# Kernel tuning notes

Measured on AMD Instinct MI355X. Metric: run time of the kernel, lower is better.

## Reference

```python
import jax, jax.numpy as jnp
import numpy as np

EMBED = 1024
HEADS = 16
HEAD_DIM = EMBED // HEADS
N, SEQ = 8, 1024


def setup_inputs() -> dict:
    key = jax.random.key(0)
    ks = jax.random.split(key, 9)
    values = jax.random.normal(ks[0], (N, SEQ, EMBED), dtype=jnp.float32)
    keys_ = jax.random.normal(ks[1], (N, SEQ, EMBED), dtype=jnp.float32)
    query = jax.random.normal(ks[2], (N, SEQ, EMBED), dtype=jnp.float32)
    mask = jax.random.randint(ks[3], (N, 1, SEQ, SEQ), 0, 2, dtype=jnp.int32)
    s = 1.0 / np.sqrt(HEAD_DIM)
    Wv = jax.random.normal(ks[4], (HEAD_DIM, HEAD_DIM), dtype=jnp.float32) * s
    Wk = jax.random.normal(ks[5], (HEAD_DIM, HEAD_DIM), dtype=jnp.float32) * s
    Wq = jax.random.normal(ks[6], (HEAD_DIM, HEAD_DIM), dtype=jnp.float32) * s
    Wo = jax.random.normal(ks[7], (EMBED, EMBED), dtype=jnp.float32) * (1.0 / np.sqrt(EMBED))
    bo = jax.random.normal(ks[8], (EMBED,), dtype=jnp.float32) * 0.01
    return {"values": values, "keys": keys_, "query": query, "mask": mask,
            "Wv": Wv, "Wk": Wk, "Wq": Wq, "Wo": Wo, "bo": bo}


def reference(values, keys, query, mask, Wv, Wk, Wq, Wo, bo):
    n, q_len = query.shape[0], query.shape[1]
    v_len, k_len = values.shape[1], keys.shape[1]
    # reshape to (N, len, H, Dh); per-head linear projections share a (Dh,Dh) weight.
    v = values.reshape(n, v_len, HEADS, HEAD_DIM)
    k = keys.reshape(n, k_len, HEADS, HEAD_DIM)
    q = query.reshape(n, q_len, HEADS, HEAD_DIM)
    # torch Linear: x @ W.T
    v = jnp.einsum('nlhd,ed->nlhe', v, Wv)
    k = jnp.einsum('nlhd,ed->nlhe', k, Wk)
    q = jnp.einsum('nlhd,ed->nlhe', q, Wq)
    # scores (N,H,Q,K); mask BEFORE scaling, exactly as the torch module does
    att = jnp.einsum('nqhd,nkhd->nhqk', q, k)
    att = jnp.where(mask == 0, jnp.float32(-1e20), att)
    att = jax.nn.softmax(att / jnp.sqrt(jnp.float32(EMBED)), axis=3)
    out = jnp.einsum('nhql,nlhd->nqhd', att, v).reshape(n, q_len, EMBED)
    return out @ Wo.T + bo
```

## Files before the change

kernel.cpp:

```cpp
#include <hip/hip_runtime.h>
#include <hip/hip_bf16.h>

using bf16x8 = __attribute__((ext_vector_type(8))) __bf16;
using f32x4  = __attribute__((ext_vector_type(4))) float;

#define NB 8
#define SEQ 1024
#define HEADS 16
#define HD 64
#define EMB 1024

#if __has_builtin(__builtin_amdgcn_exp2f)
  #define EXPD(x) __builtin_amdgcn_exp2f(x)
  #define QSCALE  0.04508422f
  #define MASKV  -4.5084e18f
#else
  #define EXPD(x) __expf(x)
  #define QSCALE  0.03125f
  #define MASKV  -3.125e18f
#endif

__global__ __launch_bounds__(256) void mask_pack(const int* __restrict__ mask,
                                                 unsigned long long* __restrict__ mp)
{
    const int row = blockIdx.x, n = blockIdx.y, t = threadIdx.x;
    const int w = t >> 6, lane = t & 63;
    const int* m = mask + ((size_t)n * SEQ + row) * SEQ;
    #pragma unroll
    for (int i = 0; i < 4; ++i) {
        unsigned long long b = __ballot(m[i * 256 + w * 64 + lane] != 0);
        if (lane == 0) mp[((size_t)n * SEQ + row) * 16 + i * 4 + w] = b;
    }
}

__global__ __launch_bounds__(256, 4) void proj_mfma(
    const float* __restrict__ q_in, const float* __restrict__ k_in, const float* __restrict__ v_in,
    const float* __restrict__ Wq, const float* __restrict__ Wk, const float* __restrict__ Wv,
    __bf16* __restrict__ qp, __bf16* __restrict__ kp, __bf16* __restrict__ vpt)
{
    const int z = blockIdx.z;
    const float* X  = (z == 0) ? q_in : (z == 1) ? k_in : v_in;
    const float* Wf = (z == 0) ? Wq   : (z == 1) ? Wk   : Wv;

    __shared__ __align__(16) __bf16 Wb[64 * 72];
    __shared__ __align__(16) __bf16 Xb[64 * 72];
    const int t = threadIdx.x;
    const int nh = blockIdx.y, n = nh >> 4, h = nh & 15;
    const int l0 = blockIdx.x * 64;
    for (int i = t; i < 4096; i += 256)
        Wb[(i >> 6) * 72 + (i & 63)] = (__bf16)Wf[i];
    {
        const int row = t >> 2, seg = (t & 3) * 16;
        const float* src = X + ((size_t)(n * SEQ + l0 + row)) * EMB + h * 64 + seg;
        union { __bf16 b[16]; uint4 u[2]; } tmp;
        #pragma unroll
        for (int jj = 0; jj < 4; ++jj) {
            float4 f = ((const float4*)src)[jj];
            tmp.b[jj*4+0] = (__bf16)f.x; tmp.b[jj*4+1] = (__bf16)f.y;
            tmp.b[jj*4+2] = (__bf16)f.z; tmp.b[jj*4+3] = (__bf16)f.w;
        }
        *(uint4*)&Xb[row * 72 + seg]     = tmp.u[0];
        *(uint4*)&Xb[row * 72 + seg + 8] = tmp.u[1];
    }
    __syncthreads();
    const int w = t >> 6, lane = t & 63, quad = lane >> 4, lr = lane & 15;
    bf16x8 af[2];
    #pragma unroll
    for (int ks = 0; ks < 2; ++ks)
        af[ks] = *(const bf16x8*)&Xb[(w * 16 + lr) * 72 + ks * 32 + quad * 8];
    const f32x4 zero4 = {0.f, 0.f, 0.f, 0.f};
    f32x4 acc[4];
    #pragma unroll
    for (int et = 0; et < 4; ++et) {
        acc[et] = zero4;
        #pragma unroll
        for (int ks = 0; ks < 2; ++ks) {
            bf16x8 bfrag = *(const bf16x8*)&Wb[(et * 16 + lr) * 72 + ks * 32 + quad * 8];
            acc[et] = __builtin_amdgcn_mfma_f32_16x16x32_bf16(af[ks], bfrag, acc[et], 0, 0, 0);
        }
    }
    if (z == 0) {
        #pragma unroll
        for (int et = 0; et < 4; ++et) acc[et] *= QSCALE;
    }
    __syncthreads();
    if (z < 2) {
        #pragma unroll
        for (int et = 0; et < 4; ++et)
            #pragma unroll
            for (int rr = 0; rr < 4; ++rr)
                Xb[(w * 16 + quad * 4 + rr) * 72 + et * 16 + lr] = (__bf16)acc[et][rr];
        __syncthreads();
        const int row = t >> 2, seg = (t & 3) * 16;
        uint4 a = *(uint4*)&Xb[row * 72 + seg];
        uint4 b = *(uint4*)&Xb[row * 72 + seg + 8];
        __bf16* outp = (z == 0) ? qp : kp;
        __bf16* dst = outp + (size_t)nh * 65536 + (size_t)(l0 + row) * 64 + seg;
        *(uint4*)&dst[0] = a;
        *(uint4*)&dst[8] = b;
    } else {
        #pragma unroll
        for (int et = 0; et < 4; ++et)
            #pragma unroll
            for (int rr = 0; rr < 4; ++rr)
                Xb[(et * 16 + lr) * 72 + w * 16 + quad * 4 + rr] = (__bf16)acc[et][rr];
        __syncthreads();
        const int e = t >> 2, seg = (t & 3) * 16;
        uint4 a = *(uint4*)&Xb[e * 72 + seg];
        uint4 b = *(uint4*)&Xb[e * 72 + seg + 8];
        __bf16* dst = vpt + (size_t)nh * 65536 + (size_t)e * SEQ + l0 + seg;
        *(uint4*)&dst[0] = a;
        *(uint4*)&dst[8] = b;
    }
}

__global__ __launch_bounds__(256, 4) void attn_mfma(
    const __bf16* __restrict__ qp, const __bf16* __restrict__ kp, const __bf16* __restrict__ vpt,
    const unsigned long long* __restrict__ mp, __bf16* __restrict__ attn_out)
{
    __shared__ __align__(16) __bf16 Ks[64 * 72];
    __shared__ __align__(16) __bf16 Vt[64 * 72];
    __shared__ __align__(16) __bf16 Ps[4][2][16 * 72];
    const int t = threadIdx.x, w = t >> 6, lane = t & 63, quad = lane >> 4, lr = lane & 15;
    const int bid = blockIdx.x;
    const int nh = bid & 127, qg = bid >> 7;
    const int n = nh >> 4, h = nh & 15;
    const int q0 = qg * 128;
    const __bf16* Q  = qp  + (size_t)nh * 65536;
    const __bf16* K  = kp  + (size_t)nh * 65536;
    const __bf16* VT = vpt + (size_t)nh * 65536;

    int qrow[2];
    bf16x8 qf[2][2];
    const unsigned long long* mrow[2];
    #pragma unroll
    for (int g = 0; g < 2; ++g) {
        qrow[g] = q0 + g * 64 + w * 16 + lr;
        qf[g][0] = *(const bf16x8*)&Q[(size_t)qrow[g] * 64 + quad * 8];
        qf[g][1] = *(const bf16x8*)&Q[(size_t)qrow[g] * 64 + 32 + quad * 8];
        mrow[g] = mp + ((size_t)n * SEQ + qrow[g]) * 16;
    }

    const f32x4 zero4 = {0.f, 0.f, 0.f, 0.f};
    f32x4 O[2][4];
    #pragma unroll
    for (int g = 0; g < 2; ++g)
        #pragma unroll
        for (int mt = 0; mt < 4; ++mt) O[g][mt] = zero4;
    float l_part[2] = {0.f, 0.f};

    for (int kc = 0; kc < 16; ++kc) {
        __syncthreads();
        for (int c = t; c < 512; c += 256) {
            int row = c >> 3, c8 = c & 7;
            *(uint4*)&Ks[row * 72 + c8 * 8] =
                *(const uint4*)&K[(size_t)(kc * 64 + row) * 64 + c8 * 8];
            *(uint4*)&Vt[row * 72 + c8 * 8] =
                *(const uint4*)&VT[(size_t)row * SEQ + kc * 64 + c8 * 8];
        }
        const unsigned long long mw0 = mrow[0][kc], mw1 = mrow[1][kc];
        __syncthreads();
        #pragma unroll
        for (int g = 0; g < 2; ++g) {
            f32x4 S[4];
            #pragma unroll
            for (int kt = 0; kt < 4; ++kt) {
                S[kt] = zero4;
                #pragma unroll
                for (int ks = 0; ks < 2; ++ks) {
                    bf16x8 kf = *(const bf16x8*)&Ks[(kt * 16 + lr) * 72 + ks * 32 + quad * 8];
                    S[kt] = __builtin_amdgcn_mfma_f32_16x16x32_bf16(kf, qf[g][ks], S[kt], 0, 0, 0);
                }
            }
            const unsigned long long mword = g ? mw1 : mw0;
            const unsigned int mlo = (unsigned int)(mword >> (quad * 4));
            const unsigned int mhi = (unsigned int)(mword >> (32 + quad * 4));
            float lsum = 0.f;
            __bf16 pb[16];
            #pragma unroll
            for (int kt = 0; kt < 4; ++kt)
                #pragma unroll
                for (int r = 0; r < 4; ++r) {
                    unsigned int bits = (kt < 2) ? mlo : mhi;
                    int sh = (kt & 1) * 16 + r;
                    float sv = ((bits >> sh) & 1u) ? S[kt][r] : MASKV;
                    float ev = EXPD(sv);
                    lsum += ev;
                    pb[kt * 4 + r] = (__bf16)ev;
                }
            l_part[g] += lsum;
            #pragma unroll
            for (int kt = 0; kt < 4; ++kt) {
                union { __bf16 b[4]; uint2 u; } pk;
                #pragma unroll
                for (int r = 0; r < 4; ++r) pk.b[r] = pb[kt * 4 + r];
                *(uint2*)&Ps[w][g][lr * 72 + kt * 16 + quad * 4] = pk.u;
            }
        }
        __asm__ __volatile__("s_waitcnt lgkmcnt(0)" ::: "memory");
        #pragma unroll
        for (int ks = 0; ks < 2; ++ks) {
            bf16x8 pf0 = *(const bf16x8*)&Ps[w][0][lr * 72 + ks * 32 + quad * 8];
            bf16x8 pf1 = *(const bf16x8*)&Ps[w][1][lr * 72 + ks * 32 + quad * 8];
            #pragma unroll
            for (int mt = 0; mt < 4; ++mt) {
                bf16x8 vf = *(const bf16x8*)&Vt[(mt * 16 + lr) * 72 + ks * 32 + quad * 8];
                O[0][mt] = __builtin_amdgcn_mfma_f32_16x16x32_bf16(vf, pf0, O[0][mt], 0, 0, 0);
                O[1][mt] = __builtin_amdgcn_mfma_f32_16x16x32_bf16(vf, pf1, O[1][mt], 0, 0, 0);
            }
        }
    }
    #pragma unroll
    for (int g = 0; g < 2; ++g) {
        float l = l_part[g];
        l += __shfl_xor(l, 16, 64);
        l += __shfl_xor(l, 32, 64);
        const float linv = 1.0f / l;
        #pragma unroll
        for (int mt = 0; mt < 4; ++mt) {
            union { __bf16 b[4]; uint2 u; } pk;
            #pragma unroll
            for (int r = 0; r < 4; ++r) pk.b[r] = (__bf16)(O[g][mt][r] * linv);
            *(uint2*)&attn_out[((size_t)n * SEQ + qrow[g]) * EMB + h * 64 + mt * 16 + quad * 4] = pk.u;
        }
    }
}

__global__ __launch_bounds__(256) void cvt_wo(const float* __restrict__ Wo, __bf16* __restrict__ Wob)
{
    int i = blockIdx.x * 256 + threadIdx.x;
    float4 f = *(const float4*)&Wo[(size_t)i * 4];
    union { __bf16 b[4]; uint2 u; } tmp;
    tmp.b[0] = (__bf16)f.x; tmp.b[1] = (__bf16)f.y; tmp.b[2] = (__bf16)f.z; tmp.b[3] = (__bf16)f.w;
    *(uint2*)&Wob[(size_t)i * 4] = tmp.u;
}

__global__ __launch_bounds__(256, 4) void out_gemm_mfma(
    const __bf16* __restrict__ A, const __bf16* __restrict__ B,
    const float* __restrict__ bo, float* __restrict__ out)
{
    __shared__ __align__(16) __bf16 As[64 * 40];
    __shared__ __align__(16) __bf16 Bs[128 * 40];
    const int t = threadIdx.x, w = t >> 6, lane = t & 63, quad = lane >> 4, lr = lane & 15;
    const int wr = (w >> 1) * 32, wc = (w & 1) * 64;
    const int r0 = blockIdx.y * 64, e0 = blockIdx.x * 128;
    const f32x4 zero4 = {0.f, 0.f, 0.f, 0.f};
    f32x4 acc[2][4];
    #pragma unroll
    for (int mt = 0; mt < 2; ++mt)
        #pragma unroll
        for (int nt = 0; nt < 4; ++nt) acc[mt][nt] = zero4;
    for (int k0 = 0; k0 < 1024; k0 += 32) {
        __syncthreads();
        {
            int row = t >> 2, c8 = t & 3;
            *(uint4*)&As[row * 40 + c8 * 8] =
                *(const uint4*)&A[(size_t)(r0 + row) * EMB + k0 + c8 * 8];
        }
        for (int c = t; c < 512; c += 256) {
            int row = c >> 2, c8 = c & 3;
            *(uint4*)&Bs[row * 40 + c8 * 8] =
                *(const uint4*)&B[(size_t)(e0 + row) * EMB + k0 + c8 * 8];
        }
        __syncthreads();
        bf16x8 af[2], bf[4];
        #pragma unroll
        for (int mt = 0; mt < 2; ++mt)
            af[mt] = *(const bf16x8*)&As[(wr + mt * 16 + lr) * 40 + quad * 8];
        #pragma unroll
        for (int nt = 0; nt < 4; ++nt)
            bf[nt] = *(const bf16x8*)&Bs[(wc + nt * 16 + lr) * 40 + quad * 8];
        #pragma unroll
        for (int mt = 0; mt < 2; ++mt)
            #pragma unroll
            for (int nt = 0; nt < 4; ++nt)
                acc[mt][nt] = __builtin_amdgcn_mfma_f32_16x16x32_bf16(af[mt], bf[nt], acc[mt][nt], 0, 0, 0);
    }
    float bv[4];
    #pragma unroll
    for (int nt = 0; nt < 4; ++nt) bv[nt] = bo[e0 + wc + nt * 16 + lr];
    #pragma unroll
    for (int mt = 0; mt < 2; ++mt)
        #pragma unroll
        for (int nt = 0; nt < 4; ++nt)
            #pragma unroll
            for (int rr = 0; rr < 4; ++rr)
                out[(size_t)(r0 + wr + mt * 16 + quad * 4 + rr) * EMB + e0 + wc + nt * 16 + lr] =
                    acc[mt][nt][rr] + bv[nt];
}

extern "C" void kernel_launch(void* const* d_in, const int* in_sizes, int n_in,
                              void* d_out, int out_size, void* d_ws, size_t ws_size,
                              hipStream_t stream) {
    const float* values = (const float*)d_in[0];
    const float* keys   = (const float*)d_in[1];
    const float* query  = (const float*)d_in[2];
    const int*   mask   = (const int*)d_in[3];
    const float* Wv     = (const float*)d_in[4];
    const float* Wk     = (const float*)d_in[5];
    const float* Wq     = (const float*)d_in[6];
    const float* Wo     = (const float*)d_in[7];
    const float* bo     = (const float*)d_in[8];
    float* out = (float*)d_out;

    const size_t per = (size_t)NB * HEADS * SEQ * HD;
    __bf16* qp   = (__bf16*)d_ws;
    __bf16* kp   = qp + per;
    __bf16* vpt  = kp + per;
    __bf16* attn = vpt + per;
    __bf16* Wob  = attn + (size_t)NB * SEQ * EMB;
    unsigned long long* maskp = (unsigned long long*)(Wob + (size_t)EMB * EMB);

    mask_pack<<<dim3(SEQ, NB), 256, 0, stream>>>(mask, maskp);
    proj_mfma<<<dim3(16, 128, 3), 256, 0, stream>>>(query, keys, values, Wq, Wk, Wv, qp, kp, vpt);
    cvt_wo<<<1024, 256, 0, stream>>>(Wo, Wob);
    attn_mfma<<<1024, 256, 0, stream>>>(qp, kp, vpt, maskp, attn);
    out_gemm_mfma<<<dim3(EMB / 128, NB * SEQ / 64), 256, 0, stream>>>(attn, Wob, bo, out);
}
```

Baseline: 284.7 us.

## Merge prep kernels, read K/V directly from global, enlarge output GEMM tile

Folds the mask-packing and Wo bf16 conversion into one launch, which removes one kernel launch. The attention kernel no longer stages K and V tiles in shared memory and drops the two block barriers per chunk. Each wave now loads its MFMA fragments straight from global memory and depends on L1/L2 for reuse across waves. The output GEMM tile grows to 128x128 with a 4x4 accumulator per wave and unpadded LDS rows. That gives more reuse per block but costs more registers, lower occupancy, and possible LDS bank conflicts.

New measurement: 351.8 us. 23.6% more time.

```diff
diff --git a/kernel.cpp b/kernel.cpp
--- a/kernel.cpp
+++ b/kernel.cpp
@@ -20,16 +20,28 @@
   #define MASKV  -3.125e18f
 #endif
 
-__global__ __launch_bounds__(256) void mask_pack(const int* __restrict__ mask,
-                                                 unsigned long long* __restrict__ mp)
+__global__ __launch_bounds__(256) void prep_kernel(const int* __restrict__ mask,
+                                                   unsigned long long* __restrict__ mp,
+                                                   const float* __restrict__ Wo,
+                                                   __bf16* __restrict__ Wob)
 {
-    const int row = blockIdx.x, n = blockIdx.y, t = threadIdx.x;
-    const int w = t >> 6, lane = t & 63;
-    const int* m = mask + ((size_t)n * SEQ + row) * SEQ;
-    #pragma unroll
-    for (int i = 0; i < 4; ++i) {
-        unsigned long long b = __ballot(m[i * 256 + w * 64 + lane] != 0);
-        if (lane == 0) mp[((size_t)n * SEQ + row) * 16 + i * 4 + w] = b;
+    const int bid = blockIdx.x, t = threadIdx.x;
+    if (bid < NB * SEQ) {
+        const int n = bid & 7, row = bid >> 3;
+        const int w = t >> 6, lane = t & 63;
+        const int* m = mask + ((size_t)n * SEQ + row) * SEQ;
+        #pragma unroll
+        for (int i = 0; i < 4; ++i) {
+            unsigned long long b = __ballot(m[i * 256 + w * 64 + lane] != 0);
+            if (lane == 0) mp[((size_t)n * SEQ + row) * 16 + i * 4 + w] = b;
+        }
+    } else {
+        const size_t i = (size_t)(bid - NB * SEQ) * 256 + t;
+        float4 f = *(const float4*)&Wo[i * 4];
+        union { __bf16 b[4]; uint2 u; } tmp;
+        tmp.b[0] = (__bf16)f.x; tmp.b[1] = (__bf16)f.y;
+        tmp.b[2] = (__bf16)f.z; tmp.b[3] = (__bf16)f.w;
+        *(uint2*)&Wob[i * 4] = tmp.u;
     }
 }
 
@@ -118,8 +130,6 @@
     const __bf16* __restrict__ qp, const __bf16* __restrict__ kp, const __bf16* __restrict__ vpt,
     const unsigned long long* __restrict__ mp, __bf16* __restrict__ attn_out)
 {
-    __shared__ __align__(16) __bf16 Ks[64 * 72];
-    __shared__ __align__(16) __bf16 Vt[64 * 72];
     __shared__ __align__(16) __bf16 Ps[4][2][16 * 72];
     const int t = threadIdx.x, w = t >> 6, lane = t & 63, quad = lane >> 4, lr = lane & 15;
     const int bid = blockIdx.x;
@@ -150,35 +160,24 @@
     float l_part[2] = {0.f, 0.f};
 
     for (int kc = 0; kc < 16; ++kc) {
-        __syncthreads();
-        for (int c = t; c < 512; c += 256) {
-            int row = c >> 3, c8 = c & 7;
-            *(uint4*)&Ks[row * 72 + c8 * 8] =
-                *(const uint4*)&K[(size_t)(kc * 64 + row) * 64 + c8 * 8];
-            *(uint4*)&Vt[row * 72 + c8 * 8] =
-                *(const uint4*)&VT[(size_t)row * SEQ + kc * 64 + c8 * 8];
-        }
-        const unsigned long long mw0 = mrow[0][kc], mw1 = mrow[1][kc];
-        __syncthreads();
         #pragma unroll
         for (int g = 0; g < 2; ++g) {
             f32x4 S[4];
             #pragma unroll
             for (int kt = 0; kt < 4; ++kt) {
-                S[kt] = zero4;
-                #pragma unroll
-                for (int ks = 0; ks < 2; ++ks) {
-                    bf16x8 kf = *(const bf16x8*)&Ks[(kt * 16 + lr) * 72 + ks * 32 + quad * 8];
-                    S[kt] = __builtin_amdgcn_mfma_f32_16x16x32_bf16(kf, qf[g][ks], S[kt], 0, 0, 0);
-                }
+                const __bf16* kb = &K[(size_t)(kc * 64 + kt * 16 + lr) * 64 + quad * 8];
+                bf16x8 kf0 = *(const bf16x8*)&kb[0];
+                bf16x8 kf1 = *(const bf16x8*)&kb[32];
+                S[kt] = __builtin_amdgcn_mfma_f32_16x16x32_bf16(kf0, qf[g][0], zero4, 0, 0, 0);
+                S[kt] = __builtin_amdgcn_mfma_f32_16x16x32_bf16(kf1, qf[g][1], S[kt], 0, 0, 0);
             }
-            const unsigned long long mword = g ? mw1 : mw0;
+            const unsigned long long mword = mrow[g][kc];
             const unsigned int mlo = (unsigned int)(mword >> (quad * 4));
             const unsigned int mhi = (unsigned int)(mword >> (32 + quad * 4));
             float lsum = 0.f;
-            __bf16 pb[16];
-            #pragma unroll
-            for (int kt = 0; kt < 4; ++kt)
+            #pragma unroll
+            for (int kt = 0; kt < 4; ++kt) {
+                union { __bf16 b[4]; uint2 u; } pk;
                 #pragma unroll
                 for (int r = 0; r < 4; ++r) {
                     unsigned int bits = (kt < 2) ? mlo : mhi;
@@ -186,16 +185,11 @@
                     float sv = ((bits >> sh) & 1u) ? S[kt][r] : MASKV;
                     float ev = EXPD(sv);
                     lsum += ev;
-                    pb[kt * 4 + r] = (__bf16)ev;
+                    pk.b[r] = (__bf16)ev;
                 }
-            l_part[g] += lsum;
-            #pragma unroll
-            for (int kt = 0; kt < 4; ++kt) {
-                union { __bf16 b[4]; uint2 u; } pk;
-                #pragma unroll
-                for (int r = 0; r < 4; ++r) pk.b[r] = pb[kt * 4 + r];
                 *(uint2*)&Ps[w][g][lr * 72 + kt * 16 + quad * 4] = pk.u;
             }
+            l_part[g] += lsum;
         }
         __asm__ __volatile__("s_waitcnt lgkmcnt(0)" ::: "memory");
         #pragma unroll
@@ -204,7 +198,7 @@
             bf16x8 pf1 = *(const bf16x8*)&Ps[w][1][lr * 72 + ks * 32 + quad * 8];
             #pragma unroll
             for (int mt = 0; mt < 4; ++mt) {
-                bf16x8 vf = *(const bf16x8*)&Vt[(mt * 16 + lr) * 72 + ks * 32 + quad * 8];
+                bf16x8 vf = *(const bf16x8*)&VT[(size_t)(mt * 16 + lr) * SEQ + kc * 64 + ks * 32 + quad * 8];
                 O[0][mt] = __builtin_amdgcn_mfma_f32_16x16x32_bf16(vf, pf0, O[0][mt], 0, 0, 0);
                 O[1][mt] = __builtin_amdgcn_mfma_f32_16x16x32_bf16(vf, pf1, O[1][mt], 0, 0, 0);
             }
@@ -226,52 +220,41 @@
     }
 }
 
-__global__ __launch_bounds__(256) void cvt_wo(const float* __restrict__ Wo, __bf16* __restrict__ Wob)
-{
-    int i = blockIdx.x * 256 + threadIdx.x;
-    float4 f = *(const float4*)&Wo[(size_t)i * 4];
-    union { __bf16 b[4]; uint2 u; } tmp;
-    tmp.b[0] = (__bf16)f.x; tmp.b[1] = (__bf16)f.y; tmp.b[2] = (__bf16)f.z; tmp.b[3] = (__bf16)f.w;
-    *(uint2*)&Wob[(size_t)i * 4] = tmp.u;
-}
-
-__global__ __launch_bounds__(256, 4) void out_gemm_mfma(
+__global__ __launch_bounds__(256, 2) void out_gemm_mfma(
     const __bf16* __restrict__ A, const __bf16* __restrict__ B,
     const float* __restrict__ bo, float* __restrict__ out)
 {
-    __shared__ __align__(16) __bf16 As[64 * 40];
-    __shared__ __align__(16) __bf16 Bs[128 * 40];
+    __shared__ __align__(16) __bf16 As[128 * 32];
+    __shared__ __align__(16) __bf16 Bs[128 * 32];
     const int t = threadIdx.x, w = t >> 6, lane = t & 63, quad = lane >> 4, lr = lane & 15;
-    const int wr = (w >> 1) * 32, wc = (w & 1) * 64;
-    const int r0 = blockIdx.y * 64, e0 = blockIdx.x * 128;
+    const int wr = (w >> 1) * 64, wc = (w & 1) * 64;
+    const int r0 = blockIdx.y * 128, e0 = blockIdx.x * 128;
     const f32x4 zero4 = {0.f, 0.f, 0.f, 0.f};
-    f32x4 acc[2][4];
-    #pragma unroll
-    for (int mt = 0; mt < 2; ++mt)
+    f32x4 acc[4][4];
+    #pragma unroll
+    for (int mt = 0; mt < 4; ++mt)
         #pragma unroll
         for (int nt = 0; nt < 4; ++nt) acc[mt][nt] = zero4;
     for (int k0 = 0; k0 < 1024; k0 += 32) {
         __syncthreads();
-        {
-            int row = t >> 2, c8 = t & 3;
-            *(uint4*)&As[row * 40 + c8 * 8] =
-                *(const uint4*)&A[(size_t)(r0 + row) * EMB + k0 + c8 * 8];
-        }
+        #pragma unroll
         for (int c = t; c < 512; c += 256) {
-            int row = c >> 2, c8 = c & 3;
-            *(uint4*)&Bs[row * 40 + c8 * 8] =
-                *(const uint4*)&B[(size_t)(e0 + row) * EMB + k0 + c8 * 8];
+            int row = c >> 2, seg = c & 3;
+            *(uint4*)&As[row * 32 + seg * 8] =
+                *(const uint4*)&A[(size_t)(r0 + row) * EMB + k0 + seg * 8];
+            *(uint4*)&Bs[row * 32 + seg * 8] =
+                *(const uint4*)&B[(size_t)(e0 + row) * EMB + k0 + seg * 8];
         }
         __syncthreads();
-        bf16x8 af[2], bf[4];
-        #pragma unroll
-        for (int mt = 0; mt < 2; ++mt)
-            af[mt] = *(const bf16x8*)&As[(wr + mt * 16 + lr) * 40 + quad * 8];
+        bf16x8 af[4], bf[4];
+        #pragma unroll
+        for (int mt = 0; mt < 4; ++mt)
+            af[mt] = *(const bf16x8*)&As[(wr + mt * 16 + lr) * 32 + quad * 8];
         #pragma unroll
         for (int nt = 0; nt < 4; ++nt)
-            bf[nt] = *(const bf16x8*)&Bs[(wc + nt * 16 + lr) * 40 + quad * 8];
-        #pragma unroll
-        for (int mt = 0; mt < 2; ++mt)
+            bf[nt] = *(const bf16x8*)&Bs[(wc + nt * 16 + lr) * 32 + quad * 8];
+        #pragma unroll
+        for (int mt = 0; mt < 4; ++mt)
             #pragma unroll
             for (int nt = 0; nt < 4; ++nt)
                 acc[mt][nt] = __builtin_amdgcn_mfma_f32_16x16x32_bf16(af[mt], bf[nt], acc[mt][nt], 0, 0, 0);
@@ -280,7 +263,7 @@
     #pragma unroll
     for (int nt = 0; nt < 4; ++nt) bv[nt] = bo[e0 + wc + nt * 16 + lr];
     #pragma unroll
-    for (int mt = 0; mt < 2; ++mt)
+    for (int mt = 0; mt < 4; ++mt)
         #pragma unroll
         for (int nt = 0; nt < 4; ++nt)
             #pragma unroll
@@ -311,9 +294,8 @@
     __bf16* Wob  = attn + (size_t)NB * SEQ * EMB;
     unsigned long long* maskp = (unsigned long long*)(Wob + (size_t)EMB * EMB);
 
-    mask_pack<<<dim3(SEQ, NB), 256, 0, stream>>>(mask, maskp);
+    prep_kernel<<<NB * SEQ + 1024, 256, 0, stream>>>(mask, maskp, Wo, Wob);
     proj_mfma<<<dim3(16, 128, 3), 256, 0, stream>>>(query, keys, values, Wq, Wk, Wv, qp, kp, vpt);
-    cvt_wo<<<1024, 256, 0, stream>>>(Wo, Wob);
     attn_mfma<<<1024, 256, 0, stream>>>(qp, kp, vpt, maskp, attn);
-    out_gemm_mfma<<<dim3(EMB / 128, NB * SEQ / 64), 256, 0, stream>>>(attn, Wob, bo, out);
-}
+    out_gemm_mfma<<<dim3(EMB / 128, NB * SEQ / 128), 256, 0, stream>>>(attn, Wob, bo, out);
+}
```
